# Optimization experiments

Measured on AMD Instinct MI355X. Metric: run time of the kernel, lower is better.

The kernel has to match this reference:

```python
import jax, jax.numpy as jnp
import numpy as np

N_SIDE = 64            # regular RBF kernel grid: 64^3 kernels
LC0_DIM = 32
CMIN, CMAX = -1.0, 1.0
COMBS = [(0, 1), (0, 2), (1, 2)]
# 2^3 cell-corner offsets for the 8 nearest regular-grid kernels
OFFS = np.array([[i, j, k] for i in (0, 1) for j in (0, 1) for k in (0, 1)], dtype=np.int32)


def grid_sample_2d(plane, coords):
    """Bilinear, align_corners=True. plane [C,H,W]; coords [N,2] in [-1,1];
    coords[:,0] indexes W, coords[:,1] indexes H (torch grid_sample convention)."""
    C, H, W = plane.shape
    x = (coords[:, 0] + 1.0) * 0.5 * (W - 1)
    y = (coords[:, 1] + 1.0) * 0.5 * (H - 1)
    x0 = jnp.clip(jnp.floor(x), 0, W - 2).astype(jnp.int32)
    y0 = jnp.clip(jnp.floor(y), 0, H - 2).astype(jnp.int32)
    wx = (x - x0)[None, :]
    wy = (y - y0)[None, :]
    p00 = plane[:, y0, x0]
    p01 = plane[:, y0, x0 + 1]
    p10 = plane[:, y0 + 1, x0]
    p11 = plane[:, y0 + 1, x0 + 1]
    out = p00 * (1 - wx) * (1 - wy) + p01 * wx * (1 - wy) + p10 * (1 - wx) * wy + p11 * wx * wy
    return out.T  # [N,C]


def rbf_features(x, lc0, ks):
    """Regular-grid kNN (8 cell corners) + inverse-quadratic RBF weighting of local codes."""
    interval = (CMAX - CMIN) / (N_SIDE - 1)
    cell = jnp.clip(jnp.floor((x - CMIN) / interval), 0, N_SIDE - 2).astype(jnp.int32)  # [N,3]
    corner = cell[:, None, :] + jnp.asarray(OFFS)[None]                                  # [N,8,3]
    idx = (corner[..., 0] * N_SIDE + corner[..., 1]) * N_SIDE + corner[..., 2]           # [N,8]
    kc = CMIN + corner.astype(x.dtype) * interval                                        # [N,8,3] kernel centers
    d2 = jnp.sum((x[:, None, :] - kc) ** 2, axis=-1)                                     # [N,8]
    s = ks[idx]                                                                          # [N,8] per-kernel shape
    phi = 1.0 / (1.0 + d2 * s * s)                                                       # ivq RBF
    phi = phi / (jnp.sum(phi, axis=-1, keepdims=True) + 1e-8)                            # rbf_lc0_normalize
    codes = lc0[idx]                                                                     # [N,8,LC0_DIM]
    return jnp.einsum('nk,nkd->nd', phi, codes)


def setup_inputs() -> dict:
    key = jax.random.key(0)
    ks_ = jax.random.split(key, 16)
    N = 524288
    aabb = jnp.array([[-1.5, -1.5, -1.5], [1.5, 1.5, 1.5]], dtype=jnp.float32)
    pts = jax.random.uniform(ks_[0], (N, 3), minval=-1.5, maxval=1.5, dtype=jnp.float32)

    def plane(k, r):  # kp_init uniform(0.1, 0.5)
        return jax.random.uniform(k, (32, r, r), minval=0.1, maxval=0.5, dtype=jnp.float32)

    resos = [128, 256, 512]
    inp = {'pts': pts, 'aabb': aabb}
    ki = 1
    for si, r in enumerate(resos):
        for ci in range(3):
            inp[f'p{si}{ci}'] = plane(ks_[ki], r)
            ki += 1
    inp['lc0'] = jax.random.uniform(ks_[ki], (N_SIDE ** 3, LC0_DIM), minval=-1e-4, maxval=1e-4, dtype=jnp.float32)
    interval = (CMAX - CMIN) / (N_SIDE - 1)
    inp['ks'] = jnp.full((N_SIDE ** 3,), 1.0 / interval, dtype=jnp.float32)  # ks_alpha=1.0
    inp['kpb'] = jax.random.uniform(ks_[ki + 1], (96 + LC0_DIM,), minval=-1e-4, maxval=1e-4, dtype=jnp.float32)
    return inp


def reference(pts, aabb, p00, p01, p02, p10, p11, p12, p20, p21, p22, lc0, ks, kpb):
    planes = [[p00, p01, p02], [p10, p11, p12], [p20, p21, p22]]
    # normalize_aabb -> [-1,1]
    x = (pts - aabb[0]) * (2.0 / (aabb[1] - aabb[0])) - 1.0
    # interpolate_ms_features: product over planes within a scale, concat across scales
    feats = []
    for scale in planes:
        interp = 1.0
        for pl, comb in zip(scale, COMBS):
            interp = interp * grid_sample_2d(pl, x[:, list(comb)])
        feats.append(interp)
    kp = jnp.concatenate(feats, axis=-1)          # [N,96]
    rbf = rbf_features(x, lc0, ks)                # [N,32]
    return jnp.concatenate([kp, rbf], axis=-1) + kpb  # [N,128], + kpb bias
```

## Files before the change

kernel.cpp:

```cpp
#include <hip/hip_runtime.h>
#include <hip/hip_bf16.h>
#include <stdint.h>

typedef __hip_bfloat16 bf16;
typedef __hip_bfloat162 bf162;

#define S0 ((size_t)(128*128*32))
#define S1 ((size_t)(256*256*32))
#define S2 ((size_t)(512*512*32))
#define LCN ((size_t)(64*64*64*32))

#define T128 (128*128/64)
#define T256 (256*256/64)
#define T512 (512*512/64)
#define TPLANES (3*T128 + 3*T256 + 3*T512)
#define TLC2 ((int)(LCN/2048))

#define NBUCKETS 32768

__device__ __forceinline__ uint32_t mpart(uint32_t x)
{
    x = (x | (x << 16)) & 0x030000FFu;
    x = (x | (x << 8))  & 0x0300F00Fu;
    x = (x | (x << 4))  & 0x030C30C3u;
    x = (x | (x << 2))  & 0x09249249u;
    return x;
}

__device__ __forceinline__ uint32_t bucket_of(float xn, float yn, float zn)
{
    float bx = fminf(fmaxf(floorf((xn + 1.0f) * 16.0f), 0.0f), 31.0f);
    float by = fminf(fmaxf(floorf((yn + 1.0f) * 16.0f), 0.0f), 31.0f);
    float bz = fminf(fmaxf(floorf((zn + 1.0f) * 16.0f), 0.0f), 31.0f);
    return mpart((uint32_t)bx) | (mpart((uint32_t)by) << 1) | (mpart((uint32_t)bz) << 2);
}

__device__ __forceinline__ uint32_t pack2(float a, float b)
{
    union { bf162 h; uint32_t u; } cv;
    cv.h = __halves2bfloat162(__float2bfloat16(a), __float2bfloat16(b));
    return cv.u;
}

__global__ __launch_bounds__(256) void zero_counts_kernel(unsigned int* __restrict__ counts)
{
    counts[blockIdx.x * 256 + threadIdx.x] = 0u;
}

__global__ __launch_bounds__(256) void prepass_kernel(
    const float* __restrict__ p00, const float* __restrict__ p01, const float* __restrict__ p02,
    const float* __restrict__ p10, const float* __restrict__ p11, const float* __restrict__ p12,
    const float* __restrict__ p20, const float* __restrict__ p21, const float* __restrict__ p22,
    const float* __restrict__ lc0,
    bf16* __restrict__ tp0, bf16* __restrict__ tp1, bf16* __restrict__ tp2,
    bf16* __restrict__ lc0b,
    const float* __restrict__ pts, const float* __restrict__ aabb,
    unsigned int* __restrict__ counts, int N)
{
    const int b = blockIdx.x;
    const int tid = threadIdx.x;
    __shared__ float t[64 * 33];
    if (b < TPLANES) {
        const float* src; bf16* dst; int HW, tile;
        if (b < 3 * T128) {
            int pid = b >> 8; tile = b & (T128 - 1); HW = 128 * 128;
            src = pid == 0 ? p00 : (pid == 1 ? p01 : p02);
            dst = tp0 + (size_t)pid * S0;
        } else if (b < 3 * T128 + 3 * T256) {
            int bb = b - 3 * T128; int pid = bb >> 10; tile = bb & (T256 - 1); HW = 256 * 256;
            src = pid == 0 ? p10 : (pid == 1 ? p11 : p12);
            dst = tp1 + (size_t)pid * S1;
        } else {
            int bb = b - 3 * T128 - 3 * T256; int pid = bb >> 12; tile = bb & (T512 - 1); HW = 512 * 512;
            src = pid == 0 ? p20 : (pid == 1 ? p21 : p22);
            dst = tp2 + (size_t)pid * S2;
        }
        const int base = tile * 64;
#pragma unroll
        for (int i = 0; i < 2; ++i) {
            int linear = i * 256 + tid;
            int ch = linear >> 4, pq = linear & 15;
            float4 v = *(const float4*)(src + (size_t)ch * HW + base + pq * 4);
            t[(pq * 4 + 0) * 33 + ch] = v.x;
            t[(pq * 4 + 1) * 33 + ch] = v.y;
            t[(pq * 4 + 2) * 33 + ch] = v.z;
            t[(pq * 4 + 3) * 33 + ch] = v.w;
        }
        __syncthreads();
        {
            int pos = tid >> 2, chunk = tid & 3;
            const float* row = t + pos * 33 + chunk * 8;
            uint4 o;
            o.x = pack2(row[0], row[1]);
            o.y = pack2(row[2], row[3]);
            o.z = pack2(row[4], row[5]);
            o.w = pack2(row[6], row[7]);
            *(uint4*)(dst + (size_t)(base + pos) * 32 + chunk * 8) = o;
        }
    } else if (b < TPLANES + TLC2) {
        size_t off = (size_t)(b - TPLANES) * 2048 + (size_t)tid * 8;
        float4 v0 = *(const float4*)(lc0 + off);
        float4 v1 = *(const float4*)(lc0 + off + 4);
        uint4 o;
        o.x = pack2(v0.x, v0.y);
        o.y = pack2(v0.z, v0.w);
        o.z = pack2(v1.x, v1.y);
        o.w = pack2(v1.z, v1.w);
        *(uint4*)(lc0b + off) = o;
    } else {
        int idx = (b - TPLANES - TLC2) * 256 + tid;
        if (idx < N) {
            float px = pts[3 * (size_t)idx + 0];
            float py = pts[3 * (size_t)idx + 1];
            float pz = pts[3 * (size_t)idx + 2];
            float xn = (px - aabb[0]) * (2.0f / (aabb[3] - aabb[0])) - 1.0f;
            float yn = (py - aabb[1]) * (2.0f / (aabb[4] - aabb[1])) - 1.0f;
            float zn = (pz - aabb[2]) * (2.0f / (aabb[5] - aabb[2])) - 1.0f;
            atomicAdd(&counts[bucket_of(xn, yn, zn)], 1u);
        }
    }
}

__global__ __launch_bounds__(1024) void scan_kernel(unsigned int* __restrict__ counts)
{
    __shared__ unsigned int sums[1024];
    const int t = threadIdx.x;
    unsigned int local[32];
    unsigned int s = 0;
#pragma unroll
    for (int i = 0; i < 32; ++i) { local[i] = counts[t * 32 + i]; s += local[i]; }
    sums[t] = s;
    __syncthreads();
    for (int off = 1; off < 1024; off <<= 1) {
        unsigned int v = (t >= off) ? sums[t - off] : 0u;
        __syncthreads();
        sums[t] += v;
        __syncthreads();
    }
    unsigned int run = sums[t] - s;
#pragma unroll
    for (int i = 0; i < 32; ++i) { unsigned int c = local[i]; counts[t * 32 + i] = run; run += c; }
}

__global__ __launch_bounds__(256) void scatter_kernel(
    const float* __restrict__ pts, const float* __restrict__ aabb,
    unsigned int* __restrict__ offsets, float4* __restrict__ sp, int N)
{
    int n = blockIdx.x * 256 + threadIdx.x;
    if (n >= N) return;
    float px = pts[3 * (size_t)n + 0];
    float py = pts[3 * (size_t)n + 1];
    float pz = pts[3 * (size_t)n + 2];
    float xn = (px - aabb[0]) * (2.0f / (aabb[3] - aabb[0])) - 1.0f;
    float yn = (py - aabb[1]) * (2.0f / (aabb[4] - aabb[1])) - 1.0f;
    float zn = (pz - aabb[2]) * (2.0f / (aabb[5] - aabb[2])) - 1.0f;
    unsigned int pos = atomicAdd(&offsets[bucket_of(xn, yn, zn)], 1u);
    float4 v; v.x = xn; v.y = yn; v.z = zn; v.w = __int_as_float(n);
    sp[pos] = v;
}

template <int R>
__device__ __forceinline__ float2 sample_tp(const bf162* __restrict__ tp,
                                            float cx, float cy, int cpair)
{
    float gx = (cx + 1.0f) * (0.5f * (float)(R - 1));
    float gy = (cy + 1.0f) * (0.5f * (float)(R - 1));
    float fx = fminf(fmaxf(floorf(gx), 0.0f), (float)(R - 2));
    float fy = fminf(fmaxf(floorf(gy), 0.0f), (float)(R - 2));
    float wx = gx - fx, wy = gy - fy;
    int ix = (int)fx, iy = (int)fy;
    int i00 = (iy * R + ix) * 16 + cpair;
    int i10 = i00 + R * 16;
    bf162 v00 = tp[i00];
    bf162 v01 = tp[i00 + 16];
    bf162 v10 = tp[i10];
    bf162 v11 = tp[i10 + 16];
    float w11 = wx * wy;
    float w01 = wx - w11;
    float w10 = wy - w11;
    float w00 = 1.0f - wx - wy + w11;
    float2 r;
    r.x = __bfloat162float(v00.x) * w00 + __bfloat162float(v01.x) * w01
        + __bfloat162float(v10.x) * w10 + __bfloat162float(v11.x) * w11;
    r.y = __bfloat162float(v00.y) * w00 + __bfloat162float(v01.y) * w01
        + __bfloat162float(v10.y) * w10 + __bfloat162float(v11.y) * w11;
    return r;
}

template <int R>
__device__ __forceinline__ float2 plane_feat(const bf162* __restrict__ tp,
                                             float xn, float yn, float zn, int cpair)
{
    const int ps = R * R * 16;
    float2 a = sample_tp<R>(tp,          xn, yn, cpair);
    float2 b = sample_tp<R>(tp + ps,     xn, zn, cpair);
    float2 c = sample_tp<R>(tp + 2 * ps, yn, zn, cpair);
    float2 r; r.x = a.x * b.x * c.x; r.y = a.y * b.y * c.y;
    return r;
}

__device__ __forceinline__ float2 sample_f32(const float* __restrict__ pl, int R,
                                             float cx, float cy, int ch)
{
    float gx = (cx + 1.0f) * 0.5f * (float)(R - 1);
    float gy = (cy + 1.0f) * 0.5f * (float)(R - 1);
    float fx = fminf(fmaxf(floorf(gx), 0.0f), (float)(R - 2));
    float fy = fminf(fmaxf(floorf(gy), 0.0f), (float)(R - 2));
    float wx = gx - fx, wy = gy - fy;
    int ix = (int)fx, iy = (int)fy;
    float w11 = wx * wy, w01 = wx - w11, w10 = wy - w11, w00 = 1.0f - wx - wy + w11;
    size_t HW = (size_t)R * R;
    const float* q0 = pl + (size_t)ch * HW + (size_t)iy * R + ix;
    const float* q1 = q0 + HW;
    float2 r;
    r.x = q0[0] * w00 + q0[1] * w01 + q0[R] * w10 + q0[R + 1] * w11;
    r.y = q1[0] * w00 + q1[1] * w01 + q1[R] * w10 + q1[R + 1] * w11;
    return r;
}

template <bool TP>
__device__ __forceinline__ float2 rbf_feat(const bf162* __restrict__ lc0b,
                                           const float* __restrict__ lc0f,
                                           const float* __restrict__ ks,
                                           float xn, float yn, float zn, int cpair)
{
    const float interval = 2.0f / 63.0f;
    const float invi = 31.5f;
    float fc0 = fminf(fmaxf(floorf((xn + 1.0f) * invi), 0.0f), 62.0f);
    float fc1 = fminf(fmaxf(floorf((yn + 1.0f) * invi), 0.0f), 62.0f);
    float fc2 = fminf(fmaxf(floorf((zn + 1.0f) * invi), 0.0f), 62.0f);
    int c0 = (int)fc0, c1 = (int)fc1, c2 = (int)fc2;
    float dx0 = xn - (-1.0f + fc0 * interval), dx1 = dx0 - interval;
    float dy0 = yn - (-1.0f + fc1 * interval), dy1 = dy0 - interval;
    float dz0 = zn - (-1.0f + fc2 * interval), dz1 = dz0 - interval;
    int ibase = (c0 * 64 + c1) * 64 + c2;

    float phi[8]; int id[8];
    float sum = 0.0f;
#pragma unroll
    for (int k = 0; k < 8; ++k) {
        int i = (k >> 2) & 1, j = (k >> 1) & 1, l = k & 1;
        int idx = ibase + i * 4096 + j * 64 + l;
        id[k] = idx;
        float ddx = i ? dx1 : dx0;
        float ddy = j ? dy1 : dy0;
        float ddz = l ? dz1 : dz0;
        float dd = ddx * ddx + ddy * ddy + ddz * ddz;
        float s = ks[idx];
        float ph = __builtin_amdgcn_rcpf(fmaf(dd, s * s, 1.0f));
        phi[k] = ph;
        sum += ph;
    }
    float inv = __builtin_amdgcn_rcpf(sum + 1e-8f);
    float ax = 0.0f, ay = 0.0f;
#pragma unroll
    for (int k = 0; k < 8; ++k) {
        float w = phi[k] * inv;
        float vx, vy;
        if (TP) {
            bf162 v = lc0b[id[k] * 16 + cpair];
            vx = __bfloat162float(v.x); vy = __bfloat162float(v.y);
        } else {
            const float* cp = lc0f + (size_t)id[k] * 32 + 2 * cpair;
            vx = cp[0]; vy = cp[1];
        }
        ax = fmaf(w, vx, ax);
        ay = fmaf(w, vy, ay);
    }
    float2 r; r.x = ax; r.y = ay;
    return r;
}

template <bool TP, bool SORTED>
__global__ __launch_bounds__(256) void field_kernel(
    const float* __restrict__ pts, const float* __restrict__ aabb,
    const float* __restrict__ p00, const float* __restrict__ p01, const float* __restrict__ p02,
    const float* __restrict__ p10, const float* __restrict__ p11, const float* __restrict__ p12,
    const float* __restrict__ p20, const float* __restrict__ p21, const float* __restrict__ p22,
    const bf162* __restrict__ tp0, const bf162* __restrict__ tp1, const bf162* __restrict__ tp2,
    const bf162* __restrict__ lc0b, const float* __restrict__ lc0f,
    const float* __restrict__ ks, const float* __restrict__ kpb,
    const float4* __restrict__ sp,
    float* __restrict__ out, int N)
{
    const int wave  = threadIdx.x >> 6;
    const int lane  = threadIdx.x & 63;
    const int p     = lane >> 4;
    const int cpair = lane & 15;
    int bid = blockIdx.x;
    if (SORTED) {
        int nb = gridDim.x;
        if ((nb & 7) == 0) bid = (bid & 7) * (nb >> 3) + (bid >> 3);
    }
    const int m = bid * 4 + p;
    if (m >= N) return;

    float xn, yn, zn;
    int n;
    if (SORTED) {
        float4 q = sp[m];
        xn = q.x; yn = q.y; zn = q.z; n = __float_as_int(q.w);
    } else {
        n = m;
        float px = pts[3 * (size_t)n + 0];
        float py = pts[3 * (size_t)n + 1];
        float pz = pts[3 * (size_t)n + 2];
        xn = (px - aabb[0]) * (2.0f / (aabb[3] - aabb[0])) - 1.0f;
        yn = (py - aabb[1]) * (2.0f / (aabb[4] - aabb[1])) - 1.0f;
        zn = (pz - aabb[2]) * (2.0f / (aabb[5] - aabb[2])) - 1.0f;
    }

    float2 val;
    int f;
    if (wave == 0) {
        if (TP) val = plane_feat<128>(tp0, xn, yn, zn, cpair);
        else {
            float2 a = sample_f32(p00, 128, xn, yn, 2 * cpair);
            float2 b = sample_f32(p01, 128, xn, zn, 2 * cpair);
            float2 c = sample_f32(p02, 128, yn, zn, 2 * cpair);
            val.x = a.x * b.x * c.x; val.y = a.y * b.y * c.y;
        }
        f = 2 * cpair;
    } else if (wave == 1) {
        if (TP) val = plane_feat<256>(tp1, xn, yn, zn, cpair);
        else {
            float2 a = sample_f32(p10, 256, xn, yn, 2 * cpair);
            float2 b = sample_f32(p11, 256, xn, zn, 2 * cpair);
            float2 c = sample_f32(p12, 256, yn, zn, 2 * cpair);
            val.x = a.x * b.x * c.x; val.y = a.y * b.y * c.y;
        }
        f = 32 + 2 * cpair;
    } else if (wave == 2) {
        if (TP) val = plane_feat<512>(tp2, xn, yn, zn, cpair);
        else {
            float2 a = sample_f32(p20, 512, xn, yn, 2 * cpair);
            float2 b = sample_f32(p21, 512, xn, zn, 2 * cpair);
            float2 c = sample_f32(p22, 512, yn, zn, 2 * cpair);
            val.x = a.x * b.x * c.x; val.y = a.y * b.y * c.y;
        }
        f = 64 + 2 * cpair;
    } else {
        val = rbf_feat<TP>(lc0b, lc0f, ks, xn, yn, zn, cpair);
        f = 96 + 2 * cpair;
    }

    val.x += kpb[f];
    val.y += kpb[f + 1];
    *(float2*)(out + (size_t)n * 128 + f) = val;
}

extern "C" void kernel_launch(void* const* d_in, const int* in_sizes, int n_in,
                              void* d_out, int out_size, void* d_ws, size_t ws_size,
                              hipStream_t stream)
{
    const float* pts  = (const float*)d_in[0];
    const float* aabb = (const float*)d_in[1];
    const float* pl[9];
    for (int i = 0; i < 9; ++i) pl[i] = (const float*)d_in[2 + i];
    const float* lc0 = (const float*)d_in[11];
    const float* ks  = (const float*)d_in[12];
    const float* kpb = (const float*)d_in[13];
    float* out = (float*)d_out;
    const int N = in_sizes[0] / 3;

    const size_t needTP = (3 * (S0 + S1 + S2) + LCN) * sizeof(bf16);
    const size_t cntOff = needTP;
    const size_t spOff  = cntOff + (size_t)NBUCKETS * 4;
    const size_t needSort = spOff + (size_t)N * 16;

    bf16* w    = (bf16*)d_ws;
    bf16* tp0  = w;
    bf16* tp1  = tp0 + 3 * S0;
    bf16* tp2  = tp1 + 3 * S1;
    bf16* lc0b = tp2 + 3 * S2;
    unsigned int* counts = (unsigned int*)((char*)d_ws + cntOff);
    float4* sp = (float4*)((char*)d_ws + spOff);

    const bool useTP   = (d_ws != nullptr) && (ws_size >= needTP);
    const bool useSort = (d_ws != nullptr) && (ws_size >= needSort);
    const int blocks = (N + 3) / 4;
    const int cntBlocks = (N + 255) / 256;

    if (useSort) {
        zero_counts_kernel<<<NBUCKETS / 256, 256, 0, stream>>>(counts);
        prepass_kernel<<<TPLANES + TLC2 + cntBlocks, 256, 0, stream>>>(
            pl[0], pl[1], pl[2], pl[3], pl[4], pl[5], pl[6], pl[7], pl[8],
            lc0, tp0, tp1, tp2, lc0b, pts, aabb, counts, N);
        scan_kernel<<<1, 1024, 0, stream>>>(counts);
        scatter_kernel<<<cntBlocks, 256, 0, stream>>>(pts, aabb, counts, sp, N);
        field_kernel<true, true><<<blocks, 256, 0, stream>>>(
            pts, aabb, pl[0], pl[1], pl[2], pl[3], pl[4], pl[5], pl[6], pl[7], pl[8],
            (const bf162*)tp0, (const bf162*)tp1, (const bf162*)tp2,
            (const bf162*)lc0b, lc0, ks, kpb, sp, out, N);
    } else if (useTP) {
        prepass_kernel<<<TPLANES + TLC2, 256, 0, stream>>>(
            pl[0], pl[1], pl[2], pl[3], pl[4], pl[5], pl[6], pl[7], pl[8],
            lc0, tp0, tp1, tp2, lc0b, pts, aabb, nullptr, 0);
        field_kernel<true, false><<<blocks, 256, 0, stream>>>(
            pts, aabb, pl[0], pl[1], pl[2], pl[3], pl[4], pl[5], pl[6], pl[7], pl[8],
            (const bf162*)tp0, (const bf162*)tp1, (const bf162*)tp2,
            (const bf162*)lc0b, lc0, ks, kpb, nullptr, out, N);
    } else {
        field_kernel<false, false><<<blocks, 256, 0, stream>>>(
            pts, aabb, pl[0], pl[1], pl[2], pl[3], pl[4], pl[5], pl[6], pl[7], pl[8],
            (const bf162*)d_ws, (const bf162*)d_ws, (const bf162*)d_ws,
            (const bf162*)d_ws, lc0, ks, kpb, nullptr, out, N);
    }
}
```

Measured before the change: 604.1 us.

## Widen field kernel to 8 channels per lane, split prepass kernels

```diff
diff --git a/kernel.cpp b/kernel.cpp
--- a/kernel.cpp
+++ b/kernel.cpp
@@ -42,80 +42,110 @@
     return cv.u;
 }
 
+__device__ __forceinline__ void unpack8(uint4 u, float* f)
+{
+    const bf162* h = (const bf162*)&u;
+    f[0] = __bfloat162float(h[0].x); f[1] = __bfloat162float(h[0].y);
+    f[2] = __bfloat162float(h[1].x); f[3] = __bfloat162float(h[1].y);
+    f[4] = __bfloat162float(h[2].x); f[5] = __bfloat162float(h[2].y);
+    f[6] = __bfloat162float(h[3].x); f[7] = __bfloat162float(h[3].y);
+}
+
 __global__ __launch_bounds__(256) void zero_counts_kernel(unsigned int* __restrict__ counts)
 {
     counts[blockIdx.x * 256 + threadIdx.x] = 0u;
 }
 
-__global__ __launch_bounds__(256) void prepass_kernel(
+__global__ __launch_bounds__(256) void transpose_kernel(
     const float* __restrict__ p00, const float* __restrict__ p01, const float* __restrict__ p02,
     const float* __restrict__ p10, const float* __restrict__ p11, const float* __restrict__ p12,
     const float* __restrict__ p20, const float* __restrict__ p21, const float* __restrict__ p22,
-    const float* __restrict__ lc0,
-    bf16* __restrict__ tp0, bf16* __restrict__ tp1, bf16* __restrict__ tp2,
-    bf16* __restrict__ lc0b,
-    const float* __restrict__ pts, const float* __restrict__ aabb,
-    unsigned int* __restrict__ counts, int N)
+    bf16* __restrict__ tp0, bf16* __restrict__ tp1, bf16* __restrict__ tp2)
 {
     const int b = blockIdx.x;
     const int tid = threadIdx.x;
     __shared__ float t[64 * 33];
-    if (b < TPLANES) {
-        const float* src; bf16* dst; int HW, tile;
-        if (b < 3 * T128) {
-            int pid = b >> 8; tile = b & (T128 - 1); HW = 128 * 128;
-            src = pid == 0 ? p00 : (pid == 1 ? p01 : p02);
-            dst = tp0 + (size_t)pid * S0;
-        } else if (b < 3 * T128 + 3 * T256) {
-            int bb = b - 3 * T128; int pid = bb >> 10; tile = bb & (T256 - 1); HW = 256 * 256;
-            src = pid == 0 ? p10 : (pid == 1 ? p11 : p12);
-            dst = tp1 + (size_t)pid * S1;
-        } else {
-            int bb = b - 3 * T128 - 3 * T256; int pid = bb >> 12; tile = bb & (T512 - 1); HW = 512 * 512;
-            src = pid == 0 ? p20 : (pid == 1 ? p21 : p22);
-            dst = tp2 + (size_t)pid * S2;
-        }
-        const int base = tile * 64;
-#pragma unroll
-        for (int i = 0; i < 2; ++i) {
-            int linear = i * 256 + tid;
-            int ch = linear >> 4, pq = linear & 15;
-            float4 v = *(const float4*)(src + (size_t)ch * HW + base + pq * 4);
-            t[(pq * 4 + 0) * 33 + ch] = v.x;
-            t[(pq * 4 + 1) * 33 + ch] = v.y;
-            t[(pq * 4 + 2) * 33 + ch] = v.z;
-            t[(pq * 4 + 3) * 33 + ch] = v.w;
-        }
-        __syncthreads();
-        {
-            int pos = tid >> 2, chunk = tid & 3;
-            const float* row = t + pos * 33 + chunk * 8;
-            uint4 o;
-            o.x = pack2(row[0], row[1]);
-            o.y = pack2(row[2], row[3]);
-            o.z = pack2(row[4], row[5]);
-            o.w = pack2(row[6], row[7]);
-            *(uint4*)(dst + (size_t)(base + pos) * 32 + chunk * 8) = o;
-        }
-    } else if (b < TPLANES + TLC2) {
-        size_t off = (size_t)(b - TPLANES) * 2048 + (size_t)tid * 8;
-        float4 v0 = *(const float4*)(lc0 + off);
-        float4 v1 = *(const float4*)(lc0 + off + 4);
+    const float* src; bf16* dst; int HW, tile;
+    if (b < 3 * T128) {
+        int pid = b >> 8; tile = b & (T128 - 1); HW = 128 * 128;
+        src = pid == 0 ? p00 : (pid == 1 ? p01 : p02);
+        dst = tp0 + (size_t)pid * S0;
+    } else if (b < 3 * T128 + 3 * T256) {
+        int bb = b - 3 * T128; int pid = bb >> 10; tile = bb & (T256 - 1); HW = 256 * 256;
+        src = pid == 0 ? p10 : (pid == 1 ? p11 : p12);
+        dst = tp1 + (size_t)pid * S1;
+    } else {
+        int bb = b - 3 * T128 - 3 * T256; int pid = bb >> 12; tile = bb & (T512 - 1); HW = 512 * 512;
+        src = pid == 0 ? p20 : (pid == 1 ? p21 : p22);
+        dst = tp2 + (size_t)pid * S2;
+    }
+    const int base = tile * 64;
+#pragma unroll
+    for (int i = 0; i < 2; ++i) {
+        int linear = i * 256 + tid;
+        int ch = linear >> 4, pq = linear & 15;
+        float4 v = *(const float4*)(src + (size_t)ch * HW + base + pq * 4);
+        t[(pq * 4 + 0) * 33 + ch] = v.x;
+        t[(pq * 4 + 1) * 33 + ch] = v.y;
+        t[(pq * 4 + 2) * 33 + ch] = v.z;
+        t[(pq * 4 + 3) * 33 + ch] = v.w;
+    }
+    __syncthreads();
+    {
+        int pos = tid >> 2, chunk = tid & 3;
+        const float* row = t + pos * 33 + chunk * 8;
         uint4 o;
-        o.x = pack2(v0.x, v0.y);
-        o.y = pack2(v0.z, v0.w);
-        o.z = pack2(v1.x, v1.y);
-        o.w = pack2(v1.z, v1.w);
-        *(uint4*)(lc0b + off) = o;
+        o.x = pack2(row[0], row[1]);
+        o.y = pack2(row[2], row[3]);
+        o.z = pack2(row[4], row[5]);
+        o.w = pack2(row[6], row[7]);
+        *(uint4*)(dst + (size_t)(base + pos) * 32 + chunk * 8) = o;
+    }
+}
+
+__global__ __launch_bounds__(256) void lc0cast_kernel(
+    const float* __restrict__ lc0, bf16* __restrict__ lc0b)
+{
+    size_t off = (size_t)blockIdx.x * 2048 + (size_t)threadIdx.x * 8;
+    float4 v0 = *(const float4*)(lc0 + off);
+    float4 v1 = *(const float4*)(lc0 + off + 4);
+    uint4 o;
+    o.x = pack2(v0.x, v0.y);
+    o.y = pack2(v0.z, v0.w);
+    o.z = pack2(v1.x, v1.y);
+    o.w = pack2(v1.z, v1.w);
+    *(uint4*)(lc0b + off) = o;
+}
+
+__global__ __launch_bounds__(256) void hist_kernel(
+    const float* __restrict__ pts, const float* __restrict__ aabb,
+    unsigned int* __restrict__ counts, int N)
+{
+    int g = blockIdx.x * 256 + threadIdx.x;
+    int b0 = g * 4;
+    if (b0 >= N) return;
+    float a0 = aabb[0], a1 = aabb[1], a2 = aabb[2];
+    float sx = 2.0f / (aabb[3] - a0);
+    float sy = 2.0f / (aabb[4] - a1);
+    float sz = 2.0f / (aabb[5] - a2);
+    if (b0 + 3 < N) {
+        const float4* p4 = (const float4*)(pts + (size_t)b0 * 3);
+        float4 A = p4[0], B = p4[1], C = p4[2];
+        float px[4] = {A.x, A.w, B.z, C.y};
+        float py[4] = {A.y, B.x, B.w, C.z};
+        float pz[4] = {A.z, B.y, C.x, C.w};
+#pragma unroll
+        for (int k = 0; k < 4; ++k) {
+            float xn = (px[k] - a0) * sx - 1.0f;
+            float yn = (py[k] - a1) * sy - 1.0f;
+            float zn = (pz[k] - a2) * sz - 1.0f;
+            atomicAdd(&counts[bucket_of(xn, yn, zn)], 1u);
+        }
     } else {
-        int idx = (b - TPLANES - TLC2) * 256 + tid;
-        if (idx < N) {
-            float px = pts[3 * (size_t)idx + 0];
-            float py = pts[3 * (size_t)idx + 1];
-            float pz = pts[3 * (size_t)idx + 2];
-            float xn = (px - aabb[0]) * (2.0f / (aabb[3] - aabb[0])) - 1.0f;
-            float yn = (py - aabb[1]) * (2.0f / (aabb[4] - aabb[1])) - 1.0f;
-            float zn = (pz - aabb[2]) * (2.0f / (aabb[5] - aabb[2])) - 1.0f;
+        for (int i = b0; i < N; ++i) {
+            float xn = (pts[3 * (size_t)i + 0] - a0) * sx - 1.0f;
+            float yn = (pts[3 * (size_t)i + 1] - a1) * sy - 1.0f;
+            float zn = (pts[3 * (size_t)i + 2] - a2) * sz - 1.0f;
             atomicAdd(&counts[bucket_of(xn, yn, zn)], 1u);
         }
     }
@@ -146,17 +176,160 @@
     const float* __restrict__ pts, const float* __restrict__ aabb,
     unsigned int* __restrict__ offsets, float4* __restrict__ sp, int N)
 {
-    int n = blockIdx.x * 256 + threadIdx.x;
-    if (n >= N) return;
-    float px = pts[3 * (size_t)n + 0];
-    float py = pts[3 * (size_t)n + 1];
-    float pz = pts[3 * (size_t)n + 2];
-    float xn = (px - aabb[0]) * (2.0f / (aabb[3] - aabb[0])) - 1.0f;
-    float yn = (py - aabb[1]) * (2.0f / (aabb[4] - aabb[1])) - 1.0f;
-    float zn = (pz - aabb[2]) * (2.0f / (aabb[5] - aabb[2])) - 1.0f;
-    unsigned int pos = atomicAdd(&offsets[bucket_of(xn, yn, zn)], 1u);
-    float4 v; v.x = xn; v.y = yn; v.z = zn; v.w = __int_as_float(n);
-    sp[pos] = v;
+    int g = blockIdx.x * 256 + threadIdx.x;
+    int b0 = g * 4;
+    if (b0 >= N) return;
+    float a0 = aabb[0], a1 = aabb[1], a2 = aabb[2];
+    float sx = 2.0f / (aabb[3] - a0);
+    float sy = 2.0f / (aabb[4] - a1);
+    float sz = 2.0f / (aabb[5] - a2);
+    if (b0 + 3 < N) {
+        const float4* p4 = (const float4*)(pts + (size_t)b0 * 3);
+        float4 A = p4[0], B = p4[1], C = p4[2];
+        float px[4] = {A.x, A.w, B.z, C.y};
+        float py[4] = {A.y, B.x, B.w, C.z};
+        float pz[4] = {A.z, B.y, C.x, C.w};
+#pragma unroll
+        for (int k = 0; k < 4; ++k) {
+            float xn = (px[k] - a0) * sx - 1.0f;
+            float yn = (py[k] - a1) * sy - 1.0f;
+            float zn = (pz[k] - a2) * sz - 1.0f;
+            unsigned int pos = atomicAdd(&offsets[bucket_of(xn, yn, zn)], 1u);
+            float4 v; v.x = xn; v.y = yn; v.z = zn; v.w = __int_as_float(b0 + k);
+            sp[pos] = v;
+        }
+    } else {
+        for (int i = b0; i < N; ++i) {
+            float xn = (pts[3 * (size_t)i + 0] - a0) * sx - 1.0f;
+            float yn = (pts[3 * (size_t)i + 1] - a1) * sy - 1.0f;
+            float zn = (pts[3 * (size_t)i + 2] - a2) * sz - 1.0f;
+            unsigned int pos = atomicAdd(&offsets[bucket_of(xn, yn, zn)], 1u);
+            float4 v; v.x = xn; v.y = yn; v.z = zn; v.w = __int_as_float(i);
+            sp[pos] = v;
+        }
+    }
+}
+
+template <int R>
+__device__ __forceinline__ void sample_tp16(const uint4* __restrict__ tq,
+                                            float cx, float cy, int cq, float* o)
+{
+    float gx = (cx + 1.0f) * (0.5f * (float)(R - 1));
+    float gy = (cy + 1.0f) * (0.5f * (float)(R - 1));
+    float fx = fminf(fmaxf(floorf(gx), 0.0f), (float)(R - 2));
+    float fy = fminf(fmaxf(floorf(gy), 0.0f), (float)(R - 2));
+    float wx = gx - fx, wy = gy - fy;
+    int ix = (int)fx, iy = (int)fy;
+    int t00 = (iy * R + ix) * 4 + cq;
+    uint4 u00 = tq[t00];
+    uint4 u01 = tq[t00 + 4];
+    uint4 u10 = tq[t00 + R * 4];
+    uint4 u11 = tq[t00 + R * 4 + 4];
+    float w11 = wx * wy;
+    float w01 = wx - w11;
+    float w10 = wy - w11;
+    float w00 = 1.0f - wx - wy + w11;
+    float a[8], b[8], c[8], d[8];
+    unpack8(u00, a); unpack8(u01, b); unpack8(u10, c); unpack8(u11, d);
+#pragma unroll
+    for (int j = 0; j < 8; ++j)
+        o[j] = a[j] * w00 + b[j] * w01 + c[j] * w10 + d[j] * w11;
+}
+
+template <int R>
+__device__ __forceinline__ void plane_feat16(const uint4* __restrict__ tq,
+                                             float xn, float yn, float zn, int cq, float* acc)
+{
+    const int ps = R * R * 4;
+    float t0[8];
+    sample_tp16<R>(tq,          xn, yn, cq, acc);
+    sample_tp16<R>(tq + ps,     xn, zn, cq, t0);
+#pragma unroll
+    for (int j = 0; j < 8; ++j) acc[j] *= t0[j];
+    sample_tp16<R>(tq + 2 * ps, yn, zn, cq, t0);
+#pragma unroll
+    for (int j = 0; j < 8; ++j) acc[j] *= t0[j];
+}
+
+__device__ __forceinline__ void rbf16(const uint4* __restrict__ lcq,
+                                      const float* __restrict__ ks,
+                                      float xn, float yn, float zn, int cq, float* acc)
+{
+    const float interval = 2.0f / 63.0f;
+    const float invi = 31.5f;
+    float fc0 = fminf(fmaxf(floorf((xn + 1.0f) * invi), 0.0f), 62.0f);
+    float fc1 = fminf(fmaxf(floorf((yn + 1.0f) * invi), 0.0f), 62.0f);
+    float fc2 = fminf(fmaxf(floorf((zn + 1.0f) * invi), 0.0f), 62.0f);
+    int c0 = (int)fc0, c1 = (int)fc1, c2 = (int)fc2;
+    float dx0 = xn - (-1.0f + fc0 * interval), dx1 = dx0 - interval;
+    float dy0 = yn - (-1.0f + fc1 * interval), dy1 = dy0 - interval;
+    float dz0 = zn - (-1.0f + fc2 * interval), dz1 = dz0 - interval;
+    int ibase = (c0 * 64 + c1) * 64 + c2;
+
+    float phi[8]; int id[8];
+    float sum = 0.0f;
+#pragma unroll
+    for (int k = 0; k < 8; ++k) {
+        int i = (k >> 2) & 1, j = (k >> 1) & 1, l = k & 1;
+        int idx = ibase + i * 4096 + j * 64 + l;
+        id[k] = idx;
+        float ddx = i ? dx1 : dx0;
+        float ddy = j ? dy1 : dy0;
+        float ddz = l ? dz1 : dz0;
+        float dd = ddx * ddx + ddy * ddy + ddz * ddz;
+        float s = ks[idx];
+        float ph = __builtin_amdgcn_rcpf(fmaf(dd, s * s, 1.0f));
+        phi[k] = ph;
+        sum += ph;
+    }
+    float inv = __builtin_amdgcn_rcpf(sum + 1e-8f);
+#pragma unroll
+    for (int j = 0; j < 8; ++j) acc[j] = 0.0f;
+#pragma unroll
+    for (int k = 0; k < 8; ++k) {
+        float w = phi[k] * inv;
+        uint4 u = lcq[id[k] * 4 + cq];
+        float v[8]; unpack8(u, v);
+#pragma unroll
+        for (int j = 0; j < 8; ++j) acc[j] = fmaf(w, v[j], acc[j]);
+    }
+}
+
+__global__ __launch_bounds__(256) void field16_kernel(
+    const uint4* __restrict__ tq0, const uint4* __restrict__ tq1, const uint4* __restrict__ tq2,
+    const uint4* __restrict__ lcq,
+    const float* __restrict__ ks, const float* __restrict__ kpb,
+    const float4* __restrict__ sp, float* __restrict__ out, int N)
+{
+    const int wave = threadIdx.x >> 6;
+    const int lane = threadIdx.x & 63;
+    const int p    = lane >> 2;
+    const int cq   = lane & 3;
+    int bid = blockIdx.x;
+    int nb = gridDim.x;
+    if ((nb & 7) == 0) bid = (bid & 7) * (nb >> 3) + (bid >> 3);
+    const int m = bid * 16 + p;
+    if (m >= N) return;
+
+    float4 q = sp[m];
+    float xn = q.x, yn = q.y, zn = q.z;
+    int n = __float_as_int(q.w);
+
+    float acc[8];
+    int base;
+    if (wave == 0)      { base = 0;  plane_feat16<128>(tq0, xn, yn, zn, cq, acc); }
+    else if (wave == 1) { base = 32; plane_feat16<256>(tq1, xn, yn, zn, cq, acc); }
+    else if (wave == 2) { base = 64; plane_feat16<512>(tq2, xn, yn, zn, cq, acc); }
+    else                { base = 96; rbf16(lcq, ks, xn, yn, zn, cq, acc); }
+
+    const float* kb = kpb + base + cq * 8;
+    float4 k0 = *(const float4*)kb;
+    float4 k1 = *(const float4*)(kb + 4);
+    float* o = out + (size_t)n * 128 + base + cq * 8;
+    float4 r0; r0.x = acc[0] + k0.x; r0.y = acc[1] + k0.y; r0.z = acc[2] + k0.z; r0.w = acc[3] + k0.w;
+    float4 r1; r1.x = acc[4] + k1.x; r1.y = acc[5] + k1.y; r1.z = acc[6] + k1.z; r1.w = acc[7] + k1.w;
+    *(float4*)o = r0;
+    *(float4*)(o + 4) = r1;
 }
 
 template <int R>
@@ -271,8 +444,8 @@
     return r;
 }
 
-template <bool TP, bool SORTED>
-__global__ __launch_bounds__(256) void field_kernel(
+template <bool TP>
+__global__ __launch_bounds__(256) void field_legacy_kernel(
     const float* __restrict__ pts, const float* __restrict__ aabb,
     const float* __restrict__ p00, const float* __restrict__ p01, const float* __restrict__ p02,
     const float* __restrict__ p10, const float* __restrict__ p11, const float* __restrict__ p12,
@@ -280,35 +453,21 @@
     const bf162* __restrict__ tp0, const bf162* __restrict__ tp1, const bf162* __restrict__ tp2,
     const bf162* __restrict__ lc0b, const float* __restrict__ lc0f,
     const float* __restrict__ ks, const float* __restrict__ kpb,
-    const float4* __restrict__ sp,
     float* __restrict__ out, int N)
 {
     const int wave  = threadIdx.x >> 6;
     const int lane  = threadIdx.x & 63;
     const int p     = lane >> 4;
     const int cpair = lane & 15;
-    int bid = blockIdx.x;
-    if (SORTED) {
-        int nb = gridDim.x;
-        if ((nb & 7) == 0) bid = (bid & 7) * (nb >> 3) + (bid >> 3);
-    }
-    const int m = bid * 4 + p;
-    if (m >= N) return;
-
-    float xn, yn, zn;
-    int n;
-    if (SORTED) {
-        float4 q = sp[m];
-        xn = q.x; yn = q.y; zn = q.z; n = __float_as_int(q.w);
-    } else {
-        n = m;
-        float px = pts[3 * (size_t)n + 0];
-        float py = pts[3 * (size_t)n + 1];
-        float pz = pts[3 * (size_t)n + 2];
-        xn = (px - aabb[0]) * (2.0f / (aabb[3] - aabb[0])) - 1.0f;
-        yn = (py - aabb[1]) * (2.0f / (aabb[4] - aabb[1])) - 1.0f;
-        zn = (pz - aabb[2]) * (2.0f / (aabb[5] - aabb[2])) - 1.0f;
-    }
+    const int n = blockIdx.x * 4 + p;
+    if (n >= N) return;
+
+    float px = pts[3 * (size_t)n + 0];
+    float py = pts[3 * (size_t)n + 1];
+    float pz = pts[3 * (size_t)n + 2];
+    float xn = (px - aabb[0]) * (2.0f / (aabb[3] - aabb[0])) - 1.0f;
+    float yn = (py - aabb[1]) * (2.0f / (aabb[4] - aabb[1])) - 1.0f;
+    float zn = (pz - aabb[2]) * (2.0f / (aabb[5] - aabb[2])) - 1.0f;
 
     float2 val;
     int f;
@@ -378,32 +537,34 @@
 
     const bool useTP   = (d_ws != nullptr) && (ws_size >= needTP);
     const bool useSort = (d_ws != nullptr) && (ws_size >= needSort);
-    const int blocks = (N + 3) / 4;
-    const int cntBlocks = (N + 255) / 256;
 
     if (useSort) {
+        const int g4 = (N + 1023) / 1024;
         zero_counts_kernel<<<NBUCKETS / 256, 256, 0, stream>>>(counts);
-        prepass_kernel<<<TPLANES + TLC2 + cntBlocks, 256, 0, stream>>>(
+        hist_kernel<<<g4, 256, 0, stream>>>(pts, aabb, counts, N);
+        transpose_kernel<<<TPLANES, 256, 0, stream>>>(
             pl[0], pl[1], pl[2], pl[3], pl[4], pl[5], pl[6], pl[7], pl[8],
-            lc0, tp0, tp1, tp2, lc0b, pts, aabb, counts, N);
+            tp0, tp1, tp2);
+        lc0cast_kernel<<<TLC2, 256, 0, stream>>>(lc0, lc0b);
         scan_kernel<<<1, 1024, 0, stream>>>(counts);
-        scatter_kernel<<<cntBlocks, 256, 0, stream>>>(pts, aabb, counts, sp, N);
-        field_kernel<true, true><<<blocks, 256, 0, stream>>>(
+        scatter_kernel<<<g4, 256, 0, stream>>>(pts, aabb, counts, sp, N);
+        const int blocks16 = (N + 15) / 16;
+        field16_kernel<<<blocks16, 256, 0, stream>>>(
+            (const uint4*)tp0, (const uint4*)tp1, (const uint4*)tp2,
+            (const uint4*)lc0b, ks, kpb, sp, out, N);
+    } else if (useTP) {
+        transpose_kernel<<<TPLANES, 256, 0, stream>>>(
+            pl[0], pl[1], pl[2], pl[3], pl[4], pl[5], pl[6], pl[7], pl[8],
+            tp0, tp1, tp2);
+        lc0cast_kernel<<<TLC2, 256, 0, stream>>>(lc0, lc0b);
+        field_legacy_kernel<true><<<(N + 3) / 4, 256, 0, stream>>>(
             pts, aabb, pl[0], pl[1], pl[2], pl[3], pl[4], pl[5], pl[6], pl[7], pl[8],
             (const bf162*)tp0, (const bf162*)tp1, (const bf162*)tp2,
-            (const bf162*)lc0b, lc0, ks, kpb, sp, out, N);
-    } else if (useTP) {
-        prepass_kernel<<<TPLANES + TLC2, 256, 0, stream>>>(
-            pl[0], pl[1], pl[2], pl[3], pl[4], pl[5], pl[6], pl[7], pl[8],
-            lc0, tp0, tp1, tp2, lc0b, pts, aabb, nullptr, 0);
-        field_kernel<true, false><<<blocks, 256, 0, stream>>>(
-            pts, aabb, pl[0], pl[1], pl[2], pl[3], pl[4], pl[5], pl[6], pl[7], pl[8],
-            (const bf162*)tp0, (const bf162*)tp1, (const bf162*)tp2,
-            (const bf162*)lc0b, lc0, ks, kpb, nullptr, out, N);
+            (const bf162*)lc0b, lc0, ks, kpb, out, N);
     } else {
-        field_kernel<false, false><<<blocks, 256, 0, stream>>>(
+        field_legacy_kernel<false><<<(N + 3) / 4, 256, 0, stream>>>(
             pts, aabb, pl[0], pl[1], pl[2], pl[3], pl[4], pl[5], pl[6], pl[7], pl[8],
             (const bf162*)d_ws, (const bf162*)d_ws, (const bf162*)d_ws,
-            (const bf162*)d_ws, lc0, ks, kpb, nullptr, out, N);
-    }
-}
+            (const bf162*)d_ws, lc0, ks, kpb, out, N);
+    }
+}
```

New measurement: 587.1 us. 1.03x faster.
